# Performance work log

Measured on AMD Instinct MI355X. Metric: run time of the kernel, lower is better.

The kernel has to match this reference:

```python
import jax, jax.numpy as jnp
import numpy as np

N = 50000          # nodes
E = 1200000        # edges (before self loops)
HID = 256          # hidden_dim
HEADS = 4
DH = HID // HEADS  # head dim = 64
SLOPE = 0.2        # PyG GATConv default negative_slope


def setup_inputs() -> dict:
    key = jax.random.key(0)
    k1, k2, k3, k4, k5 = jax.random.split(key, 5)
    x = jax.random.normal(k1, (N, HID), dtype=jnp.float32)
    # GATConv params: shared linear W, per-head attention vectors a_src/a_dst, bias
    W = jax.random.normal(k2, (HID, HEADS * DH), dtype=jnp.float32) / np.float32(np.sqrt(HID))
    att_src = jax.random.normal(k3, (HEADS, DH), dtype=jnp.float32) * 0.1
    att_dst = jax.random.normal(k4, (HEADS, DH), dtype=jnp.float32) * 0.1
    bias = jnp.zeros((HEADS * DH,), dtype=jnp.float32)
    edge_index = jax.random.randint(k5, (2, E), 0, N, dtype=jnp.int32)
    return {"x": x, "W": W, "att_src": att_src, "att_dst": att_dst,
            "bias": bias, "edge_index": edge_index}


def reference(x, W, att_src, att_dst, bias, edge_index):
    # add self loops (PyG GATConv default add_self_loops=True)
    loops = jnp.arange(N, dtype=edge_index.dtype)
    src = jnp.concatenate([edge_index[0], loops])  # message source
    dst = jnpp_dst = jnp.concatenate([edge_index[1], loops])  # message target / softmax segment

    h = (x @ W).reshape(N, HEADS, DH)                       # [N,H,D]
    a_s = jnp.einsum('nhd,hd->nh', h, att_src)              # [N,H]
    a_d = jnp.einsum('nhd,hd->nh', h, att_dst)              # [N,H]

    e = jax.nn.leaky_relu(a_s[src] + a_d[dst], SLOPE)       # [Etot,H] edge logits
    # segment-wise (per destination node) stable softmax
    emax = jax.ops.segment_max(e, dst, num_segments=N)      # [N,H]
    ez = jnp.exp(e - emax[dst])
    denom = jax.ops.segment_sum(ez, dst, num_segments=N)    # [N,H]
    alpha = ez / (denom[dst] + 1e-16)                       # [Etot,H]

    msg = h[src] * alpha[:, :, None]                        # [Etot,H,D]
    out = jax.ops.segment_sum(msg, dst, num_segments=N)     # [N,H,D]
    out = out.reshape(N, HEADS * DH) + bias                 # concat heads + bias
    return jax.nn.relu(out)
```

## Files before the change

### kernel.cpp

```cpp
#include <hip/hip_runtime.h>
#include <hip/hip_bf16.h>
#include <hip/hip_fp16.h>

#define HID 256
#define HEADS 4
#define DH 64
#define SLOPE 0.2f
#define NBMAX 512
#define BCAP 4096

typedef __attribute__((ext_vector_type(8))) _Float16 f16x8;
typedef __attribute__((ext_vector_type(4))) float f32x4;

__device__ inline float leaky(float x) { return x >= 0.f ? x : SLOPE * x; }

__global__ __launch_bounds__(256) void transpose_w(const float* __restrict__ W,
                                                   _Float16* __restrict__ Wt,
                                                   int* __restrict__ bucket_cnt) {
  int n = blockIdx.x;
  int k = threadIdx.x;
  Wt[n * HID + k] = (_Float16)W[(size_t)k * HID + n];
  if (n == 0) {
    bucket_cnt[k] = 0;
    bucket_cnt[k + 256] = 0;
  }
}

__global__ __launch_bounds__(512) void gemm_xw_f16(const float* __restrict__ X,
                                                   const _Float16* __restrict__ Wt,
                                                   const float* __restrict__ att_src,
                                                   const float* __restrict__ att_dst,
                                                   _Float16* __restrict__ Hp,
                                                   float* __restrict__ a_s,
                                                   float* __restrict__ a_d, int M) {
  __shared__ _Float16 sA[128][40];
  const int t = threadIdx.x;
  const int wave = t >> 6;
  const int l = t & 63;
  const int wm = wave >> 2;
  const int wn = wave & 3;
  const int row0 = blockIdx.x * 128;

  f32x4 acc[4][4] = {};

  for (int ks = 0; ks < 8; ++ks) {
    const int r = t >> 2;
    const int fo = (t & 3) * 8;
    const int gr = row0 + r;
    float4 v0 = make_float4(0.f, 0.f, 0.f, 0.f), v1 = v0;
    if (gr < M) {
      const float* p = X + (size_t)gr * HID + ks * 32 + fo;
      v0 = *(const float4*)p;
      v1 = *(const float4*)(p + 4);
    }
    _Float16 tmp[8] = {(_Float16)v0.x, (_Float16)v0.y, (_Float16)v0.z, (_Float16)v0.w,
                       (_Float16)v1.x, (_Float16)v1.y, (_Float16)v1.z, (_Float16)v1.w};
    __syncthreads();
    *(uint4*)&sA[r][fo] = *(uint4*)tmp;
    __syncthreads();

    f16x8 af[4];
#pragma unroll
    for (int mt = 0; mt < 4; ++mt)
      af[mt] = *(const f16x8*)&sA[wm * 64 + mt * 16 + (l & 15)][(l >> 4) * 8];
#pragma unroll
    for (int nt = 0; nt < 4; ++nt) {
      const f16x8 bfr = *(const f16x8*)(Wt + (size_t)(wn * 64 + nt * 16 + (l & 15)) * HID
                                        + ks * 32 + (l >> 4) * 8);
#pragma unroll
      for (int mt = 0; mt < 4; ++mt)
        acc[mt][nt] = __builtin_amdgcn_mfma_f32_16x16x32_f16(af[mt], bfr, acc[mt][nt], 0, 0, 0);
    }
  }

  const int head = wn;
  float as_v[4], ad_v[4];
#pragma unroll
  for (int nt = 0; nt < 4; ++nt) {
    as_v[nt] = att_src[head * DH + nt * 16 + (l & 15)];
    ad_v[nt] = att_dst[head * DH + nt * 16 + (l & 15)];
  }
#pragma unroll
  for (int mt = 0; mt < 4; ++mt) {
#pragma unroll
    for (int reg = 0; reg < 4; ++reg) {
      float ps = 0.f, pd = 0.f;
#pragma unroll
      for (int nt = 0; nt < 4; ++nt) {
        ps += acc[mt][nt][reg] * as_v[nt];
        pd += acc[mt][nt][reg] * ad_v[nt];
      }
#pragma unroll
      for (int off = 1; off < 16; off <<= 1) {
        ps += __shfl_xor(ps, off, 64);
        pd += __shfl_xor(pd, off, 64);
      }
      const int row = row0 + wm * 64 + mt * 16 + (l >> 4) * 4 + reg;
      if ((l & 15) == 0 && row < M) {
        a_s[(size_t)head * M + row] = ps;
        a_d[(size_t)head * M + row] = pd;
      }
    }
  }

#pragma unroll
  for (int mt = 0; mt < 4; ++mt) {
    const int rbase = row0 + wm * 64 + mt * 16 + (l >> 4) * 4;
#pragma unroll
    for (int nt = 0; nt < 4; ++nt) {
      const int dh = nt * 16 + (l & 15);
#pragma unroll
      for (int reg = 0; reg < 4; ++reg) {
        const int row = rbase + reg;
        if (row < M)
          Hp[((size_t)head * M + row) * DH + dh] = (_Float16)acc[mt][nt][reg];
      }
    }
  }
}

__global__ __launch_bounds__(256) void bucket_hist(const int* __restrict__ ei, int E, int Etot,
                                                   int* __restrict__ bucket_cnt, int NB) {
  __shared__ int h[NBMAX];
  for (int i = threadIdx.x; i < NB; i += 256) h[i] = 0;
  __syncthreads();
  const int g0 = blockIdx.x * 1024;
#pragma unroll
  for (int j = 0; j < 4; ++j) {
    const int e0 = (g0 + j * 256 + threadIdx.x) * 4;
    if (e0 >= Etot) continue;
    if (e0 >= E) {
#pragma unroll
      for (int k = 0; k < 4; ++k) atomicAdd(&h[(e0 - E + k) >> 7], 1);
    } else {
      const int4 d4 = *(const int4*)(ei + E + e0);
      atomicAdd(&h[d4.x >> 7], 1);
      atomicAdd(&h[d4.y >> 7], 1);
      atomicAdd(&h[d4.z >> 7], 1);
      atomicAdd(&h[d4.w >> 7], 1);
    }
  }
  __syncthreads();
  for (int i = threadIdx.x; i < NB; i += 256)
    if (h[i]) atomicAdd(&bucket_cnt[i], h[i]);
}

__global__ __launch_bounds__(512) void scan_buckets(const int* __restrict__ bucket_cnt,
                                                    int* __restrict__ bucket_base,
                                                    int* __restrict__ bucket_cursor,
                                                    int* __restrict__ offsets,
                                                    int Nn, int Etot, int NB) {
  __shared__ int h[512];
  const int tid = threadIdx.x;
  const int v = (tid < NB) ? bucket_cnt[tid] : 0;
  h[tid] = v;
  __syncthreads();
#pragma unroll
  for (int off = 1; off < 512; off <<= 1) {
    const int t = (tid >= off) ? h[tid - off] : 0;
    __syncthreads();
    h[tid] += t;
    __syncthreads();
  }
  if (tid < NB) {
    const int base = h[tid] - v;
    bucket_base[tid] = base;
    bucket_cursor[tid] = base;
  }
  if (tid == 0) offsets[Nn] = Etot;
}

__global__ __launch_bounds__(256) void scatter_tmp(const int* __restrict__ ei, int E, int Etot,
                                                   int* __restrict__ bucket_cursor,
                                                   unsigned* __restrict__ tmp, int NB) {
  __shared__ int h[NBMAX];
  __shared__ int cur[NBMAX];
  for (int i = threadIdx.x; i < NB; i += 256) h[i] = 0;
  __syncthreads();
  const int g0 = blockIdx.x * 1024;
#pragma unroll
  for (int j = 0; j < 4; ++j) {
    const int e0 = (g0 + j * 256 + threadIdx.x) * 4;
    if (e0 >= Etot) continue;
    if (e0 >= E) {
#pragma unroll
      for (int k = 0; k < 4; ++k) atomicAdd(&h[(e0 - E + k) >> 7], 1);
    } else {
      const int4 d4 = *(const int4*)(ei + E + e0);
      atomicAdd(&h[d4.x >> 7], 1);
      atomicAdd(&h[d4.y >> 7], 1);
      atomicAdd(&h[d4.z >> 7], 1);
      atomicAdd(&h[d4.w >> 7], 1);
    }
  }
  __syncthreads();
  for (int i = threadIdx.x; i < NB; i += 256)
    cur[i] = h[i] ? atomicAdd(&bucket_cursor[i], h[i]) : 0;
  __syncthreads();
#pragma unroll
  for (int j = 0; j < 4; ++j) {
    const int e0 = (g0 + j * 256 + threadIdx.x) * 4;
    if (e0 >= Etot) continue;
    int s[4], dn[4];
    if (e0 >= E) {
#pragma unroll
      for (int k = 0; k < 4; ++k) { s[k] = e0 - E + k; dn[k] = s[k]; }
    } else {
      const int4 s4 = *(const int4*)(ei + e0);
      const int4 d4 = *(const int4*)(ei + E + e0);
      s[0] = s4.x; s[1] = s4.y; s[2] = s4.z; s[3] = s4.w;
      dn[0] = d4.x; dn[1] = d4.y; dn[2] = d4.z; dn[3] = d4.w;
    }
#pragma unroll
    for (int k = 0; k < 4; ++k) {
      const int b = dn[k] >> 7;
      const int pos = atomicAdd(&cur[b], 1);
      tmp[pos] = (unsigned)s[k] | ((unsigned)(dn[k] & 127) << 16);
    }
  }
}

__global__ __launch_bounds__(256) void csr_build(const unsigned* __restrict__ tmp,
                                                 const int* __restrict__ bucket_base,
                                                 const int* __restrict__ bucket_cursor,
                                                 int* __restrict__ offsets,
                                                 int* __restrict__ csr_src, int Nn) {
  __shared__ int h[128], cur[128];
  __shared__ int cs[BCAP];
  const int b = blockIdx.x;
  const int start = bucket_base[b];
  const int cnt = min(bucket_cursor[b] - start, BCAP);
  const int tid = threadIdx.x;
  if (tid < 128) h[tid] = 0;
  __syncthreads();
  for (int i = tid; i < cnt; i += 256)
    atomicAdd(&h[tmp[start + i] >> 16], 1);
  __syncthreads();
  const int own = (tid < 128) ? h[tid] : 0;
#pragma unroll
  for (int off = 1; off < 128; off <<= 1) {
    const int t = (tid < 128 && tid >= off) ? h[tid - off] : 0;
    __syncthreads();
    if (tid < 128) h[tid] += t;
    __syncthreads();
  }
  if (tid < 128) {
    const int excl = h[tid] - own;
    cur[tid] = excl;
    const int n = b * 128 + tid;
    if (n < Nn) offsets[n] = start + excl;
  }
  __syncthreads();
  for (int i = tid; i < cnt; i += 256) {
    const unsigned p = tmp[start + i];
    const int pos = atomicAdd(&cur[p >> 16], 1);
    cs[pos] = (int)(p & 0xffffu);
  }
  __syncthreads();
  for (int i = tid; i < cnt; i += 256)
    csr_src[start + i] = cs[i];
}

__global__ __launch_bounds__(256) void gat_agg2(const int* __restrict__ offsets,
                                                const int* __restrict__ csr_src,
                                                const float* __restrict__ a_s,
                                                const float* __restrict__ a_d,
                                                const _Float16* __restrict__ Hp,
                                                const float* __restrict__ bias,
                                                float* __restrict__ out, int Nn, int nbNode) {
  const int head = blockIdx.x / nbNode;
  const int nb   = blockIdx.x - head * nbNode;
  const int wave = threadIdx.x >> 6;
  const int lane = threadIdx.x & 63;
  const int half = lane >> 5;
  const int hl   = lane & 31;
  const int g2   = hl >> 3;
  const int sl   = hl & 7;
  const int n    = nb * 8 + wave * 2 + half;

  int start = 0, end = 0;
  if (n < Nn) { start = offsets[n]; end = offsets[n + 1]; }
  const float* __restrict__ as_h = a_s + (size_t)head * Nn;
  const float adn = (n < Nn) ? a_d[(size_t)head * Nn + n] : 0.f;
  const _Float16* __restrict__ Hh = Hp + (size_t)head * Nn * DH + sl * 8;

  float m = -INFINITY, l = 0.f;
  __half2 acc[4];
#pragma unroll
  for (int j = 0; j < 4; ++j) acc[j] = __float2half2_rn(0.f);

  const int nChunk = (end - start + 31) >> 5;
  for (int c = 0; c < nChunk; ++c) {
    const int base = start + c * 32;
    const int cnt = min(32, end - base);
    const int idx = min(base + hl, end - 1);
    const int src = csr_src[idx];
    const float lg = leaky(as_h[src] + adn);
    const float logit = (hl < cnt) ? lg : -INFINITY;

    float cm = logit;
#pragma unroll
    for (int off = 16; off > 0; off >>= 1) cm = fmaxf(cm, __shfl_xor(cm, off, 64));
    const float nm = fmaxf(m, cm);
    const float scale = __expf(m - nm);
    const __half2 s2 = __float2half2_rn(scale);
#pragma unroll
    for (int j = 0; j < 4; ++j) acc[j] = __hmul2(acc[j], s2);
    l *= scale;
    const float p = __expf(logit - nm);
    float psum = p;
#pragma unroll
    for (int off = 16; off > 0; off >>= 1) psum += __shfl_xor(psum, off, 64);
    l += psum;
    m = nm;

    const unsigned combo = (unsigned)src |
                           ((unsigned)__half_as_ushort(__float2half(p)) << 16);
    const int nIt = (cnt + 3) >> 2;
#pragma unroll 4
    for (int i = 0; i < nIt; ++i) {
      const int e = i * 4 + g2;
      const unsigned cc = (unsigned)__shfl((int)combo, half * 32 + e, 64);
      const unsigned se = cc & 0xffffu;
      const __half ah = __ushort_as_half((unsigned short)(cc >> 16));
      const __half2 a2 = __halves2half2(ah, ah);
      const uint4 hv = *(const uint4*)(Hh + (size_t)se * DH);
      acc[0] = __hfma2(a2, *(const __half2*)&hv.x, acc[0]);
      acc[1] = __hfma2(a2, *(const __half2*)&hv.y, acc[1]);
      acc[2] = __hfma2(a2, *(const __half2*)&hv.z, acc[2]);
      acc[3] = __hfma2(a2, *(const __half2*)&hv.w, acc[3]);
    }
  }
#pragma unroll
  for (int off = 8; off <= 16; off <<= 1)
#pragma unroll
    for (int j = 0; j < 4; ++j) {
      int tbits = __shfl_xor(*(const int*)&acc[j], off, 64);
      acc[j] = __hadd2(acc[j], *(const __half2*)&tbits);
    }

  if (hl < 8 && n < Nn) {
    const float inv = 1.f / (l + 1e-16f);
    float v[8];
#pragma unroll
    for (int j = 0; j < 4; ++j) {
      v[2 * j]     = __low2float(acc[j]);
      v[2 * j + 1] = __high2float(acc[j]);
    }
#pragma unroll
    for (int j = 0; j < 8; ++j)
      v[j] = fmaxf(v[j] * inv + bias[head * DH + sl * 8 + j], 0.f);
    float* op = out + (size_t)n * HID + head * DH + sl * 8;
    *(float4*)op = make_float4(v[0], v[1], v[2], v[3]);
    *(float4*)(op + 4) = make_float4(v[4], v[5], v[6], v[7]);
  }
}

extern "C" void kernel_launch(void* const* d_in, const int* in_sizes, int n_in,
                              void* d_out, int out_size, void* d_ws, size_t ws_size,
                              hipStream_t stream) {
  const float* x       = (const float*)d_in[0];
  const float* Wm      = (const float*)d_in[1];
  const float* att_src = (const float*)d_in[2];
  const float* att_dst = (const float*)d_in[3];
  const float* bias    = (const float*)d_in[4];
  const int*   ei      = (const int*)d_in[5];

  const int Nn   = in_sizes[0] / HID;
  const int E    = in_sizes[5] / 2;
  const int Etot = E + Nn;
  const int NB   = (Nn + 127) >> 7;

  float* out = (float*)d_out;

  _Float16* Hp    = (_Float16*)d_ws;
  _Float16* Wt    = Hp + (size_t)HEADS * Nn * DH;
  float* a_s      = (float*)(Wt + HID * HID);
  float* a_d      = a_s + (size_t)HEADS * Nn;
  int*   offsets  = (int*)(a_d + (size_t)HEADS * Nn);
  int*   bucket_cnt    = offsets + (Nn + 1);
  int*   bucket_base   = bucket_cnt + NBMAX;
  int*   bucket_cursor = bucket_base + NBMAX;
  unsigned* tmp   = (unsigned*)(bucket_cursor + NBMAX);
  int*   csr_src  = (int*)(tmp + Etot);

  const int nbNode = (Nn + 7) / 8;
  const int nbEdge = (Etot + 4095) / 4096;

  transpose_w<<<HID, HID, 0, stream>>>(Wm, Wt, bucket_cnt);
  gemm_xw_f16<<<(Nn + 127) / 128, 512, 0, stream>>>(x, Wt, att_src, att_dst,
                                                    Hp, a_s, a_d, Nn);

  bucket_hist<<<nbEdge, 256, 0, stream>>>(ei, E, Etot, bucket_cnt, NB);
  scan_buckets<<<1, 512, 0, stream>>>(bucket_cnt, bucket_base, bucket_cursor,
                                      offsets, Nn, Etot, NB);
  scatter_tmp<<<nbEdge, 256, 0, stream>>>(ei, E, Etot, bucket_cursor, tmp, NB);
  csr_build<<<NB, 256, 0, stream>>>(tmp, bucket_base, bucket_cursor,
                                    offsets, csr_src, Nn);
  gat_agg2<<<HEADS * nbNode, 256, 0, stream>>>(offsets, csr_src, a_s, a_d, Hp, bias,
                                               out, Nn, nbNode);
}
```

Baseline: 176.1 us.

## Replace LDS-staged GEMM with direct-load 32-row tiles per block

The X·W GEMM no longer stages X through shared memory with barriers. Each wave now loads its A fragments straight from global memory and converts them to fp16. Each block covers 32 rows with four waves, one per head, instead of 128 rows with eight waves. This removes the LDS traffic and the __syncthreads and launches many more, smaller blocks. In exchange, every wave redundantly loads the same X rows (4x reuse loss across heads) and each B fragment is reused over fewer rows.

```diff
diff --git a/kernel.cpp b/kernel.cpp
--- a/kernel.cpp
+++ b/kernel.cpp
@@ -26,62 +26,54 @@
   }
 }
 
-__global__ __launch_bounds__(512) void gemm_xw_f16(const float* __restrict__ X,
+__global__ __launch_bounds__(256) void gemm_direct(const float* __restrict__ X,
                                                    const _Float16* __restrict__ Wt,
                                                    const float* __restrict__ att_src,
                                                    const float* __restrict__ att_dst,
                                                    _Float16* __restrict__ Hp,
                                                    float* __restrict__ a_s,
                                                    float* __restrict__ a_d, int M) {
-  __shared__ _Float16 sA[128][40];
-  const int t = threadIdx.x;
-  const int wave = t >> 6;
-  const int l = t & 63;
-  const int wm = wave >> 2;
-  const int wn = wave & 3;
-  const int row0 = blockIdx.x * 128;
-
-  f32x4 acc[4][4] = {};
+  const int head = threadIdx.x >> 6;
+  const int l = threadIdx.x & 63;
+  const int row0 = blockIdx.x * 32;
+  const int lr = l & 15;
+  const int lk = l >> 4;
+
+  f32x4 acc[2][4] = {};
 
   for (int ks = 0; ks < 8; ++ks) {
-    const int r = t >> 2;
-    const int fo = (t & 3) * 8;
-    const int gr = row0 + r;
-    float4 v0 = make_float4(0.f, 0.f, 0.f, 0.f), v1 = v0;
-    if (gr < M) {
-      const float* p = X + (size_t)gr * HID + ks * 32 + fo;
-      v0 = *(const float4*)p;
-      v1 = *(const float4*)(p + 4);
-    }
-    _Float16 tmp[8] = {(_Float16)v0.x, (_Float16)v0.y, (_Float16)v0.z, (_Float16)v0.w,
-                       (_Float16)v1.x, (_Float16)v1.y, (_Float16)v1.z, (_Float16)v1.w};
-    __syncthreads();
-    *(uint4*)&sA[r][fo] = *(uint4*)tmp;
-    __syncthreads();
-
-    f16x8 af[4];
-#pragma unroll
-    for (int mt = 0; mt < 4; ++mt)
-      af[mt] = *(const f16x8*)&sA[wm * 64 + mt * 16 + (l & 15)][(l >> 4) * 8];
+    f16x8 af[2];
+#pragma unroll
+    for (int mt = 0; mt < 2; ++mt) {
+      const int row = row0 + mt * 16 + lr;
+      float4 v0 = make_float4(0.f, 0.f, 0.f, 0.f), v1 = v0;
+      if (row < M) {
+        const float* p = X + (size_t)row * HID + ks * 32 + lk * 8;
+        v0 = *(const float4*)p;
+        v1 = *(const float4*)(p + 4);
+      }
+      _Float16 tmp[8] = {(_Float16)v0.x, (_Float16)v0.y, (_Float16)v0.z, (_Float16)v0.w,
+                         (_Float16)v1.x, (_Float16)v1.y, (_Float16)v1.z, (_Float16)v1.w};
+      af[mt] = *(const f16x8*)tmp;
+    }
 #pragma unroll
     for (int nt = 0; nt < 4; ++nt) {
-      const f16x8 bfr = *(const f16x8*)(Wt + (size_t)(wn * 64 + nt * 16 + (l & 15)) * HID
-                                        + ks * 32 + (l >> 4) * 8);
-#pragma unroll
-      for (int mt = 0; mt < 4; ++mt)
+      const f16x8 bfr = *(const f16x8*)(Wt + (size_t)(head * 64 + nt * 16 + lr) * HID
+                                        + ks * 32 + lk * 8);
+#pragma unroll
+      for (int mt = 0; mt < 2; ++mt)
         acc[mt][nt] = __builtin_amdgcn_mfma_f32_16x16x32_f16(af[mt], bfr, acc[mt][nt], 0, 0, 0);
     }
   }
 
-  const int head = wn;
   float as_v[4], ad_v[4];
 #pragma unroll
   for (int nt = 0; nt < 4; ++nt) {
-    as_v[nt] = att_src[head * DH + nt * 16 + (l & 15)];
-    ad_v[nt] = att_dst[head * DH + nt * 16 + (l & 15)];
-  }
-#pragma unroll
-  for (int mt = 0; mt < 4; ++mt) {
+    as_v[nt] = att_src[head * DH + nt * 16 + lr];
+    ad_v[nt] = att_dst[head * DH + nt * 16 + lr];
+  }
+#pragma unroll
+  for (int mt = 0; mt < 2; ++mt) {
 #pragma unroll
     for (int reg = 0; reg < 4; ++reg) {
       float ps = 0.f, pd = 0.f;
@@ -95,8 +87,8 @@
         ps += __shfl_xor(ps, off, 64);
         pd += __shfl_xor(pd, off, 64);
       }
-      const int row = row0 + wm * 64 + mt * 16 + (l >> 4) * 4 + reg;
-      if ((l & 15) == 0 && row < M) {
+      const int row = row0 + mt * 16 + lk * 4 + reg;
+      if (lr == 0 && row < M) {
         a_s[(size_t)head * M + row] = ps;
         a_d[(size_t)head * M + row] = pd;
       }
@@ -104,14 +96,13 @@
   }
 
 #pragma unroll
-  for (int mt = 0; mt < 4; ++mt) {
-    const int rbase = row0 + wm * 64 + mt * 16 + (l >> 4) * 4;
+  for (int mt = 0; mt < 2; ++mt) {
 #pragma unroll
     for (int nt = 0; nt < 4; ++nt) {
-      const int dh = nt * 16 + (l & 15);
+      const int dh = nt * 16 + lr;
 #pragma unroll
       for (int reg = 0; reg < 4; ++reg) {
-        const int row = rbase + reg;
+        const int row = row0 + mt * 16 + lk * 4 + reg;
         if (row < M)
           Hp[((size_t)head * M + row) * DH + dh] = (_Float16)acc[mt][nt][reg];
       }
@@ -388,8 +379,8 @@
   const int nbEdge = (Etot + 4095) / 4096;
 
   transpose_w<<<HID, HID, 0, stream>>>(Wm, Wt, bucket_cnt);
-  gemm_xw_f16<<<(Nn + 127) / 128, 512, 0, stream>>>(x, Wt, att_src, att_dst,
-                                                    Hp, a_s, a_d, Nn);
+  gemm_direct<<<(Nn + 31) / 32, 256, 0, stream>>>(x, Wt, att_src, att_dst,
+                                                  Hp, a_s, a_d, Nn);
 
   bucket_hist<<<nbEdge, 256, 0, stream>>>(ei, E, Etot, bucket_cnt, NB);
   scan_buckets<<<1, 512, 0, stream>>>(bucket_cnt, bucket_base, bucket_cursor,
```

Result: slower. 197.0 us (+11.9%).
